# Kernel tuning notes

Hardware: AMD Instinct MI355X
Metric: run time of the kernel (lower is better)

The kernel has to match this reference:

```python
import jax, jax.numpy as jnp
import numpy as np

N_NODES = 100000
N_EDGES = 1600000


def gcn_conv(x, src, dst, W, b, n_nodes):
    # PyG GCNConv: h = x @ W; symmetric normalization with self-loops; scatter-add; + bias
    deg = jax.ops.segment_sum(jnp.ones_like(src, dtype=x.dtype), dst, num_segments=n_nodes)
    dinv = jax.lax.rsqrt(jnp.where(deg > 0, deg, 1.0))
    norm = dinv[src] * dinv[dst]              # [E+N]
    h = x @ W                                  # [N, out]
    msg = h[src] * norm[:, None]               # gather + scale (irregular access)
    out = jax.ops.segment_sum(msg, dst, num_segments=n_nodes)  # scatter-add aggregate
    return out + b


def setup_inputs() -> dict:
    key = jax.random.key(0)
    k1, k2, k3, k4 = jax.random.split(key, 4)
    x = jax.random.normal(k1, (N_NODES, 128), dtype=jnp.float32)
    edge_index = jax.random.randint(k2, (2, N_EDGES), 0, N_NODES, dtype=jnp.int64)
    W1 = jax.random.normal(k3, (128, 48), dtype=jnp.float32) * (1.0 / np.sqrt(128))
    b1 = jnp.zeros((48,), dtype=jnp.float32)
    W2 = jax.random.normal(k4, (48, 16), dtype=jnp.float32) * (1.0 / np.sqrt(48))
    b2 = jnp.zeros((16,), dtype=jnp.float32)
    return {"x": x, "edge_index": edge_index, "W1": W1, "b1": b1, "W2": W2, "b2": b2}


def reference(x, edge_index, W1, b1, W2, b2):
    n = x.shape[0]
    loops = jnp.arange(n, dtype=edge_index.dtype)
    src = jnp.concatenate([edge_index[0], loops])  # add self-loops
    dst = jnp.concatenate([edge_index[1], loops])
    h = gcn_conv(x, src, dst, W1, b1, n)
    h = jax.nn.relu(h)
    h = gcn_conv(h, src, dst, W2, b2, n)
    h = jax.nn.relu(h)
    return jax.nn.softmax(h, axis=1)
```

## Files before the change

### kernel.cpp

```cpp
#include <hip/hip_runtime.h>
#include <hip/hip_bf16.h>
#include <hip/hip_fp16.h>


#define TILE 4096

typedef _Float16 half8 __attribute__((ext_vector_type(8)));
typedef float floatx4 __attribute__((ext_vector_type(4)));

__global__ __launch_bounds__(256) void k_bhist(const int* __restrict__ dst, int E,
                                               int* __restrict__ Hw, int nbuck) {
    __shared__ int h[512];
    int t = threadIdx.x;
    for (int i = t; i < nbuck; i += 256) h[i] = 0;
    __syncthreads();
    int base = blockIdx.x * TILE;
#pragma unroll
    for (int r = 0; r < TILE / 256; ++r) {
        int e = base + r * 256 + t;
        if (e < E) atomicAdd(&h[dst[e] >> 8], 1);
    }
    __syncthreads();
    for (int i = t; i < nbuck; i += 256) Hw[blockIdx.x * nbuck + i] = h[i];
}

__global__ __launch_bounds__(256) void k_bsum(const int* __restrict__ Hw, int nTiles,
                                              int nbuck, int* __restrict__ btot) {
    int wid = (blockIdx.x * 256 + threadIdx.x) >> 6;
    int lane = threadIdx.x & 63;
    if (wid >= nbuck) return;
    int sum = 0;
    for (int tt = lane; tt < nTiles; tt += 64) sum += Hw[tt * nbuck + wid];
#pragma unroll
    for (int off = 32; off; off >>= 1) sum += __shfl_down(sum, off);
    if (lane == 0) btot[wid] = sum;
}

__global__ __launch_bounds__(512) void k_bscan2(const int* __restrict__ btot, int nbuck,
                                                int* __restrict__ bstart) {
    __shared__ int s[512];
    int t = threadIdx.x;
    int v = (t < nbuck) ? btot[t] : 0;
    s[t] = v;
    __syncthreads();
    for (int off = 1; off < 512; off <<= 1) {
        int tmp = (t >= off) ? s[t - off] : 0;
        __syncthreads();
        s[t] += tmp;
        __syncthreads();
    }
    if (t < nbuck) bstart[t] = s[t] - v;
    if (t == nbuck - 1) bstart[nbuck] = s[t];
}

__global__ __launch_bounds__(256) void k_boff(int* __restrict__ Hw, int nTiles,
                                              int nbuck, const int* __restrict__ bstart) {
    int wid = (blockIdx.x * 256 + threadIdx.x) >> 6;
    int lane = threadIdx.x & 63;
    if (wid >= nbuck) return;
    int running = bstart[wid];
    for (int chunk = 0; chunk < nTiles; chunk += 64) {
        int tt = chunk + lane;
        int v = (tt < nTiles) ? Hw[tt * nbuck + wid] : 0;
        int incl = v;
#pragma unroll
        for (int off = 1; off < 64; off <<= 1) {
            int u = __shfl_up(incl, off);
            if (lane >= off) incl += u;
        }
        if (tt < nTiles) Hw[tt * nbuck + wid] = running + (incl - v);
        running += __shfl(incl, 63);
    }
}

__global__ __launch_bounds__(256) void k_bscatter(const int* __restrict__ ei, int E,
                                                  const int* __restrict__ Hw, int nbuck,
                                                  int* __restrict__ ebuf) {
    __shared__ int cur[512];
    int t = threadIdx.x;
    for (int i = t; i < nbuck; i += 256) cur[i] = Hw[blockIdx.x * nbuck + i];
    __syncthreads();
    int base = blockIdx.x * TILE;
#pragma unroll
    for (int r = 0; r < TILE / 256; ++r) {
        int e = base + r * 256 + t;
        if (e < E) {
            int s = ei[e];
            int d = ei[E + e];
            int pos = atomicAdd(&cur[d >> 8], 1);
            ebuf[pos] = s | ((d & 255) << 17);
        }
    }
}

__global__ __launch_bounds__(256) void k_csrfill(const int* __restrict__ ebuf,
                                                 const int* __restrict__ bstart,
                                                 int* __restrict__ csr,
                                                 int* __restrict__ rowstart,
                                                 float* __restrict__ dinv, int N) {
    __shared__ int lcnt[256];
    __shared__ int lscan[256];
    __shared__ int lcur[256];
    int t = threadIdx.x;
    int nodebase = blockIdx.x << 8;
    int segs = bstart[blockIdx.x];
    int sege = bstart[blockIdx.x + 1];
    lcnt[t] = 0;
    __syncthreads();
    for (int i = segs + t; i < sege; i += 256)
        atomicAdd(&lcnt[((unsigned)ebuf[i]) >> 17], 1);
    __syncthreads();
    int v = lcnt[t];
    lscan[t] = v;
    __syncthreads();
    for (int off = 1; off < 256; off <<= 1) {
        int tmp = (t >= off) ? lscan[t - off] : 0;
        __syncthreads();
        lscan[t] += tmp;
        __syncthreads();
    }
    int excl = lscan[t] - v;
    int node = nodebase + t;
    int rs = segs + excl;
    if (node < N) {
        rowstart[node] = rs;
        dinv[node] = rsqrtf((float)(v + 1));
        if (node == N - 1) rowstart[N] = rs + v;
    }
    lcur[t] = rs;
    __syncthreads();
    for (int i = segs + t; i < sege; i += 256) {
        int pk = ebuf[i];
        int pos = atomicAdd(&lcur[((unsigned)pk) >> 17], 1);
        csr[pos] = pk & 0x1FFFF;
    }
}

__global__ __launch_bounds__(256) void k_gemm1(const float* __restrict__ x,
                                               const float* __restrict__ W1,
                                               const float* __restrict__ dinv,
                                               __half* __restrict__ h1p, int N) {
    __shared__ _Float16 wt[48 * 136];
    int t = threadIdx.x;
    for (int i = t; i < 128 * 48; i += 256) {
        int k = i / 48, c = i % 48;
        wt[c * 136 + k] = (_Float16)W1[i];
    }
    __syncthreads();

    int wave = t >> 6, lane = t & 63;
    int g = lane >> 4;
    int rtile = blockIdx.x * 64 + wave * 16;
    int rowA = rtile + (lane & 15);
    const float* xrow = x + (size_t)(rowA < N ? rowA : N - 1) * 128;
    int c0 = lane & 15;

    floatx4 acc[3];
#pragma unroll
    for (int nt = 0; nt < 3; ++nt)
#pragma unroll
        for (int q = 0; q < 4; ++q) acc[nt][q] = 0.f;

#pragma unroll
    for (int kc = 0; kc < 4; ++kc) {
        int k0 = kc * 32 + g * 8;
        float4 a0 = *(const float4*)(xrow + k0);
        float4 a1 = *(const float4*)(xrow + k0 + 4);
        half8 a;
        a[0] = (_Float16)a0.x; a[1] = (_Float16)a0.y;
        a[2] = (_Float16)a0.z; a[3] = (_Float16)a0.w;
        a[4] = (_Float16)a1.x; a[5] = (_Float16)a1.y;
        a[6] = (_Float16)a1.z; a[7] = (_Float16)a1.w;
#pragma unroll
        for (int nt = 0; nt < 3; ++nt) {
            half8 b = *(const half8*)(&wt[(nt * 16 + c0) * 136 + k0]);
            acc[nt] = __builtin_amdgcn_mfma_f32_16x16x32_f16(a, b, acc[nt], 0, 0, 0);
        }
    }

    int rbase = rtile + g * 4;
#pragma unroll
    for (int j = 0; j < 4; ++j) {
        int r = rbase + j;
        if (r < N) {
            float dr = dinv[r];
#pragma unroll
            for (int nt = 0; nt < 3; ++nt)
                h1p[(size_t)r * 48 + nt * 16 + c0] = __float2half(acc[nt][j] * dr);
        }
    }
}

__global__ __launch_bounds__(256) void k_agg1(const __half* __restrict__ h1p,
                                              const int* __restrict__ csr,
                                              const int* __restrict__ rowstart,
                                              const float* __restrict__ dinv,
                                              const float* __restrict__ b1,
                                              __half* __restrict__ r1h, int N) {
    int wave = threadIdx.x >> 6;
    int lane = threadIdx.x & 63;
    int v = blockIdx.x * 4 + wave;
    if (v >= N) return;
    int grp = lane >> 3;
    int sub = lane & 7;

    int start = rowstart[v];
    int d = rowstart[v + 1] - start;
    float dv = dinv[v];
    const int* cs = csr + start;
    const char* h1b = (const char*)h1p;

    float acc[8] = {0.f, 0.f, 0.f, 0.f, 0.f, 0.f, 0.f, 0.f};

    for (int base = 0; base < d; base += 64) {
        int sreg = (base + lane < d) ? cs[base + lane] : 0;
        int nb = min(64, d - base);
        for (int j = 0; j < 8 && j * 8 < nb; ++j) {
            int s = __shfl(sreg, j * 8 + grp);
            if (j * 8 + grp < nb && sub < 6) {
                float4 rv = *(const float4*)(h1b + (size_t)s * 96 + sub * 16);
                const __half2* hp = (const __half2*)&rv;
#pragma unroll
                for (int q = 0; q < 4; ++q) {
                    float2 f = __half22float2(hp[q]);
                    acc[q * 2] += f.x;
                    acc[q * 2 + 1] += f.y;
                }
            }
        }
    }
#pragma unroll
    for (int i = 0; i < 8; ++i) {
        acc[i] += __shfl_xor(acc[i], 8);
        acc[i] += __shfl_xor(acc[i], 16);
        acc[i] += __shfl_xor(acc[i], 32);
    }
    if (grp == 0 && sub < 6) {
        float4 sv = *(const float4*)(h1b + (size_t)v * 96 + sub * 16);
        const __half2* hp = (const __half2*)&sv;
        __half2 ob[4];
#pragma unroll
        for (int q = 0; q < 4; ++q) {
            float2 sf = __half22float2(hp[q]);
            int fi = sub * 8 + q * 2;
            float o0 = fmaxf(dv * (acc[q * 2] + sf.x) + b1[fi], 0.f);
            float o1 = fmaxf(dv * (acc[q * 2 + 1] + sf.y) + b1[fi + 1], 0.f);
            ob[q] = __floats2half2_rn(o0, o1);
        }
        *(float4*)((char*)r1h + (size_t)v * 96 + sub * 16) = *(const float4*)ob;
    }
}

__global__ __launch_bounds__(256) void k_gemm2(const __half* __restrict__ r1h,
                                               const float* __restrict__ W2,
                                               const float* __restrict__ dinv,
                                               __half* __restrict__ h2p, int N) {
    __shared__ float w2s[48 * 16];
    int t = threadIdx.x;
    for (int i = t; i < 768; i += 256) w2s[i] = W2[i];
    __syncthreads();
    int flat = blockIdx.x * 256 + t;
    int row = flat >> 2;
    int cg = (flat & 3) * 4;
    if (row >= N) return;
    float4 acc = make_float4(0.f, 0.f, 0.f, 0.f);
    const __half2* xr = (const __half2*)((const char*)r1h + (size_t)row * 96);
#pragma unroll 4
    for (int kk = 0; kk < 24; ++kk) {
        float2 a = __half22float2(xr[kk]);
        float4 b0 = *(const float4*)(w2s + (2 * kk) * 16 + cg);
        float4 b1v = *(const float4*)(w2s + (2 * kk + 1) * 16 + cg);
        acc.x += a.x * b0.x + a.y * b1v.x;
        acc.y += a.x * b0.y + a.y * b1v.y;
        acc.z += a.x * b0.z + a.y * b1v.z;
        acc.w += a.x * b0.w + a.y * b1v.w;
    }
    float dr = dinv[row];
    __half2 h01 = __floats2half2_rn(acc.x * dr, acc.y * dr);
    __half2 h23 = __floats2half2_rn(acc.z * dr, acc.w * dr);
    __half* dst = h2p + (size_t)row * 16 + cg;
    *(__half2*)(dst) = h01;
    *(__half2*)(dst + 2) = h23;
}

__global__ __launch_bounds__(256) void k_agg2(const __half* __restrict__ h2p,
                                              const int* __restrict__ csr,
                                              const int* __restrict__ rowstart,
                                              const float* __restrict__ dinv,
                                              const float* __restrict__ b2,
                                              float* __restrict__ out, int N) {
    int tid = threadIdx.x;
    int lane = tid & 63;
    int hf = lane >> 5;
    int l32 = lane & 31;
    int grp = l32 >> 1;
    int sub = lane & 1;
    int v = (blockIdx.x * 4 + (tid >> 6)) * 2 + hf;
    if (v >= N) return;

    int start = rowstart[v];
    int d = rowstart[v + 1] - start;
    float dv = dinv[v];
    const int* cs = csr + start;
    const char* h2b = (const char*)h2p;

    float acc[8] = {0.f, 0.f, 0.f, 0.f, 0.f, 0.f, 0.f, 0.f};

    for (int base = 0; base < d; base += 32) {
        int sreg = (base + l32 < d) ? cs[base + l32] : 0;
        int nb = min(32, d - base);
#pragma unroll
        for (int j = 0; j < 2; ++j) {
            int e = j * 16 + grp;
            int s = __shfl(sreg, (hf << 5) + e);
            if (e < nb) {
                float4 rv = *(const float4*)(h2b + (size_t)s * 32 + sub * 16);
                const __half2* hp = (const __half2*)&rv;
#pragma unroll
                for (int q = 0; q < 4; ++q) {
                    float2 f = __half22float2(hp[q]);
                    acc[q * 2] += f.x;
                    acc[q * 2 + 1] += f.y;
                }
            }
        }
    }
#pragma unroll
    for (int i = 0; i < 8; ++i) {
        acc[i] += __shfl_xor(acc[i], 2);
        acc[i] += __shfl_xor(acc[i], 4);
        acc[i] += __shfl_xor(acc[i], 8);
        acc[i] += __shfl_xor(acc[i], 16);
    }
    if (grp == 0) {
        float4 sv = *(const float4*)(h2b + (size_t)v * 32 + sub * 16);
        const __half2* hp = (const __half2*)&sv;
        float z[8];
#pragma unroll
        for (int q = 0; q < 4; ++q) {
            float2 f = __half22float2(hp[q]);
            z[q * 2]     = fmaxf(dv * (acc[q * 2] + f.x) + b2[sub * 8 + q * 2], 0.f);
            z[q * 2 + 1] = fmaxf(dv * (acc[q * 2 + 1] + f.y) + b2[sub * 8 + q * 2 + 1], 0.f);
        }
        float m8 = z[0];
#pragma unroll
        for (int i = 1; i < 8; ++i) m8 = fmaxf(m8, z[i]);
        float m = fmaxf(m8, __shfl_xor(m8, 1));
        float p[8];
        float s8 = 0.f;
#pragma unroll
        for (int i = 0; i < 8; ++i) { p[i] = __expf(z[i] - m); s8 += p[i]; }
        float inv = 1.f / (s8 + __shfl_xor(s8, 1));
        float4* dst = (float4*)(out + (size_t)v * 16 + sub * 8);
        dst[0] = make_float4(p[0] * inv, p[1] * inv, p[2] * inv, p[3] * inv);
        dst[1] = make_float4(p[4] * inv, p[5] * inv, p[6] * inv, p[7] * inv);
    }
}

extern "C" void kernel_launch(void* const* d_in, const int* in_sizes, int n_in,
                              void* d_out, int out_size, void* d_ws, size_t ws_size,
                              hipStream_t stream) {
    const float* x  = (const float*)d_in[0];
    const int*   ei = (const int*)d_in[1];
    const float* W1 = (const float*)d_in[2];
    const float* b1 = (const float*)d_in[3];
    const float* W2 = (const float*)d_in[4];
    const float* b2 = (const float*)d_in[5];
    float* out = (float*)d_out;

    int N = in_sizes[0] / 128;
    int E = in_sizes[1] / 2;
    int NBK = (N + 255) >> 8;
    int nTiles = (E + TILE - 1) / TILE;

    char* p = (char*)d_ws;
    auto alloc = [&](size_t bytes) -> char* {
        char* q = p;
        p += (bytes + 255) & ~(size_t)255;
        return q;
    };
    int*    rowstart = (int*)alloc((size_t)(N + 1) * 4);
    float*  dinv     = (float*)alloc((size_t)N * 4);
    int*    btot     = (int*)alloc((size_t)NBK * 4);
    int*    bstart   = (int*)alloc((size_t)(NBK + 1) * 4);
    int*    Hw       = (int*)alloc((size_t)nTiles * NBK * 4);
    int*    csr      = (int*)alloc((size_t)E * 4);
    size_t  ovl_sz   = (size_t)N * 48 * 2 > (size_t)E * 4 ? (size_t)N * 48 * 2
                                                          : (size_t)E * 4;
    char*   ovl      = alloc(ovl_sz);
    int*    ebuf     = (int*)ovl;
    __half* h1p      = (__half*)ovl;
    __half* r1h      = (__half*)alloc((size_t)N * 48 * 2);
    __half* h2p      = h1p;

    int wgBuck = (NBK + 3) / 4;

    hipLaunchKernelGGL(k_bhist, dim3(nTiles), dim3(256), 0, stream, ei + E, E, Hw, NBK);
    hipLaunchKernelGGL(k_bsum, dim3(wgBuck), dim3(256), 0, stream, Hw, nTiles, NBK, btot);
    hipLaunchKernelGGL(k_bscan2, dim3(1), dim3(512), 0, stream, btot, NBK, bstart);
    hipLaunchKernelGGL(k_boff, dim3(wgBuck), dim3(256), 0, stream, Hw, nTiles, NBK, bstart);
    hipLaunchKernelGGL(k_bscatter, dim3(nTiles), dim3(256), 0, stream, ei, E, Hw, NBK, ebuf);
    hipLaunchKernelGGL(k_csrfill, dim3(NBK), dim3(256), 0, stream,
                       ebuf, bstart, csr, rowstart, dinv, N);
    hipLaunchKernelGGL(k_gemm1, dim3((N + 63) / 64), dim3(256), 0, stream,
                       x, W1, dinv, h1p, N);
    hipLaunchKernelGGL(k_agg1, dim3((N + 3) / 4), dim3(256), 0, stream,
                       h1p, csr, rowstart, dinv, b1, r1h, N);
    hipLaunchKernelGGL(k_gemm2, dim3((N * 4 + 255) / 256), dim3(256), 0, stream,
                       r1h, W2, dinv, h2p, N);
    hipLaunchKernelGGL(k_agg2, dim3((N + 7) / 8), dim3(256), 0, stream,
                       h2p, csr, rowstart, dinv, b2, out, N);
}
```

Measured before the change: 143.7 us.

## Fuse layer-1 aggregation with layer-2 GEMM and fold bucket scan into offsets

Merges k_agg1 and k_gemm2 into one kernel. Each wave aggregates a node's 48-wide row, stages the ReLU output in shared memory and multiplies it by W2 straight away, so the r1h intermediate never goes to global memory and one launch disappears. h1p rows are padded from 48 to 64 halves (128 bytes) so all eight lanes of a gather group load aligned 16-byte chunks without the sub<6 mask. The padding raises gather traffic per neighbor by a third. The single-block k_bscan2 is removed: each k_boff wave now computes its own bucket prefix by summing btot, which adds redundant reads in exchange for one fewer launch.

```diff
diff --git a/kernel.cpp b/kernel.cpp
--- a/kernel.cpp
+++ b/kernel.cpp
@@ -36,29 +36,22 @@
     if (lane == 0) btot[wid] = sum;
 }
 
-__global__ __launch_bounds__(512) void k_bscan2(const int* __restrict__ btot, int nbuck,
-                                                int* __restrict__ bstart) {
-    __shared__ int s[512];
-    int t = threadIdx.x;
-    int v = (t < nbuck) ? btot[t] : 0;
-    s[t] = v;
-    __syncthreads();
-    for (int off = 1; off < 512; off <<= 1) {
-        int tmp = (t >= off) ? s[t - off] : 0;
-        __syncthreads();
-        s[t] += tmp;
-        __syncthreads();
-    }
-    if (t < nbuck) bstart[t] = s[t] - v;
-    if (t == nbuck - 1) bstart[nbuck] = s[t];
-}
-
 __global__ __launch_bounds__(256) void k_boff(int* __restrict__ Hw, int nTiles,
-                                              int nbuck, const int* __restrict__ bstart) {
+                                              int nbuck, const int* __restrict__ btot,
+                                              int* __restrict__ bstart) {
     int wid = (blockIdx.x * 256 + threadIdx.x) >> 6;
     int lane = threadIdx.x & 63;
     if (wid >= nbuck) return;
-    int running = bstart[wid];
+    int ps = 0;
+    for (int j = lane; j < wid; j += 64) ps += btot[j];
+#pragma unroll
+    for (int off = 32; off; off >>= 1) ps += __shfl_down(ps, off);
+    int prefix = __shfl(ps, 0);
+    if (lane == 0) {
+        bstart[wid] = prefix;
+        if (wid == nbuck - 1) bstart[nbuck] = prefix + btot[wid];
+    }
+    int running = prefix;
     for (int chunk = 0; chunk < nTiles; chunk += 64) {
         int tt = chunk + lane;
         int v = (tt < nTiles) ? Hw[tt * nbuck + wid] : 0;
@@ -186,101 +179,88 @@
             float dr = dinv[r];
 #pragma unroll
             for (int nt = 0; nt < 3; ++nt)
-                h1p[(size_t)r * 48 + nt * 16 + c0] = __float2half(acc[nt][j] * dr);
-        }
-    }
-}
-
-__global__ __launch_bounds__(256) void k_agg1(const __half* __restrict__ h1p,
-                                              const int* __restrict__ csr,
-                                              const int* __restrict__ rowstart,
-                                              const float* __restrict__ dinv,
-                                              const float* __restrict__ b1,
-                                              __half* __restrict__ r1h, int N) {
-    int wave = threadIdx.x >> 6;
-    int lane = threadIdx.x & 63;
+                h1p[(size_t)r * 64 + nt * 16 + c0] = __float2half(acc[nt][j] * dr);
+            h1p[(size_t)r * 64 + 48 + c0] = __float2half(0.f);
+        }
+    }
+}
+
+__global__ __launch_bounds__(256) void k_agg1f(const __half* __restrict__ h1p,
+                                               const int* __restrict__ csr,
+                                               const int* __restrict__ rowstart,
+                                               const float* __restrict__ dinv,
+                                               const float* __restrict__ b1,
+                                               const float* __restrict__ W2,
+                                               __half* __restrict__ h2p, int N) {
+    __shared__ float w2s[48 * 16];
+    __shared__ float r1s[4][48];
+    int t = threadIdx.x;
+    for (int i = t; i < 768; i += 256) w2s[i] = W2[i];
+
+    int wave = t >> 6;
+    int lane = t & 63;
     int v = blockIdx.x * 4 + wave;
-    if (v >= N) return;
+    bool active = v < N;
     int grp = lane >> 3;
     int sub = lane & 7;
 
-    int start = rowstart[v];
-    int d = rowstart[v + 1] - start;
-    float dv = dinv[v];
+    int start = 0, d = 0;
+    float dv = 0.f;
+    if (active) {
+        start = rowstart[v];
+        d = rowstart[v + 1] - start;
+        dv = dinv[v];
+    }
     const int* cs = csr + start;
     const char* h1b = (const char*)h1p;
 
     float acc[8] = {0.f, 0.f, 0.f, 0.f, 0.f, 0.f, 0.f, 0.f};
 
-    for (int base = 0; base < d; base += 64) {
-        int sreg = (base + lane < d) ? cs[base + lane] : 0;
-        int nb = min(64, d - base);
-        for (int j = 0; j < 8 && j * 8 < nb; ++j) {
-            int s = __shfl(sreg, j * 8 + grp);
-            if (j * 8 + grp < nb && sub < 6) {
-                float4 rv = *(const float4*)(h1b + (size_t)s * 96 + sub * 16);
-                const __half2* hp = (const __half2*)&rv;
-#pragma unroll
-                for (int q = 0; q < 4; ++q) {
-                    float2 f = __half22float2(hp[q]);
-                    acc[q * 2] += f.x;
-                    acc[q * 2 + 1] += f.y;
+    if (active) {
+        for (int base = 0; base < d; base += 64) {
+            int sreg = (base + lane < d) ? cs[base + lane] : 0;
+            int nb = min(64, d - base);
+#pragma unroll
+            for (int j = 0; j < 8; ++j) {
+                int e = j * 8 + grp;
+                int s = __shfl(sreg, e);
+                if (e < nb) {
+                    float4 rv = *(const float4*)(h1b + (size_t)s * 128 + sub * 16);
+                    const __half2* hp = (const __half2*)&rv;
+#pragma unroll
+                    for (int q = 0; q < 4; ++q) {
+                        float2 f = __half22float2(hp[q]);
+                        acc[q * 2] += f.x;
+                        acc[q * 2 + 1] += f.y;
+                    }
                 }
             }
         }
-    }
-#pragma unroll
-    for (int i = 0; i < 8; ++i) {
-        acc[i] += __shfl_xor(acc[i], 8);
-        acc[i] += __shfl_xor(acc[i], 16);
-        acc[i] += __shfl_xor(acc[i], 32);
-    }
-    if (grp == 0 && sub < 6) {
-        float4 sv = *(const float4*)(h1b + (size_t)v * 96 + sub * 16);
-        const __half2* hp = (const __half2*)&sv;
-        __half2 ob[4];
-#pragma unroll
-        for (int q = 0; q < 4; ++q) {
-            float2 sf = __half22float2(hp[q]);
-            int fi = sub * 8 + q * 2;
-            float o0 = fmaxf(dv * (acc[q * 2] + sf.x) + b1[fi], 0.f);
-            float o1 = fmaxf(dv * (acc[q * 2 + 1] + sf.y) + b1[fi + 1], 0.f);
-            ob[q] = __floats2half2_rn(o0, o1);
-        }
-        *(float4*)((char*)r1h + (size_t)v * 96 + sub * 16) = *(const float4*)ob;
-    }
-}
-
-__global__ __launch_bounds__(256) void k_gemm2(const __half* __restrict__ r1h,
-                                               const float* __restrict__ W2,
-                                               const float* __restrict__ dinv,
-                                               __half* __restrict__ h2p, int N) {
-    __shared__ float w2s[48 * 16];
-    int t = threadIdx.x;
-    for (int i = t; i < 768; i += 256) w2s[i] = W2[i];
-    __syncthreads();
-    int flat = blockIdx.x * 256 + t;
-    int row = flat >> 2;
-    int cg = (flat & 3) * 4;
-    if (row >= N) return;
-    float4 acc = make_float4(0.f, 0.f, 0.f, 0.f);
-    const __half2* xr = (const __half2*)((const char*)r1h + (size_t)row * 96);
-#pragma unroll 4
-    for (int kk = 0; kk < 24; ++kk) {
-        float2 a = __half22float2(xr[kk]);
-        float4 b0 = *(const float4*)(w2s + (2 * kk) * 16 + cg);
-        float4 b1v = *(const float4*)(w2s + (2 * kk + 1) * 16 + cg);
-        acc.x += a.x * b0.x + a.y * b1v.x;
-        acc.y += a.x * b0.y + a.y * b1v.y;
-        acc.z += a.x * b0.z + a.y * b1v.z;
-        acc.w += a.x * b0.w + a.y * b1v.w;
-    }
-    float dr = dinv[row];
-    __half2 h01 = __floats2half2_rn(acc.x * dr, acc.y * dr);
-    __half2 h23 = __floats2half2_rn(acc.z * dr, acc.w * dr);
-    __half* dst = h2p + (size_t)row * 16 + cg;
-    *(__half2*)(dst) = h01;
-    *(__half2*)(dst + 2) = h23;
+#pragma unroll
+        for (int i = 0; i < 8; ++i) {
+            acc[i] += __shfl_xor(acc[i], 8);
+            acc[i] += __shfl_xor(acc[i], 16);
+            acc[i] += __shfl_xor(acc[i], 32);
+        }
+        if (grp == 0 && sub < 6) {
+            float4 sv = *(const float4*)(h1b + (size_t)v * 128 + sub * 16);
+            const __half2* hp = (const __half2*)&sv;
+#pragma unroll
+            for (int q = 0; q < 4; ++q) {
+                float2 sf = __half22float2(hp[q]);
+                int fi = sub * 8 + q * 2;
+                r1s[wave][fi]     = fmaxf(dv * (acc[q * 2] + sf.x) + b1[fi], 0.f);
+                r1s[wave][fi + 1] = fmaxf(dv * (acc[q * 2 + 1] + sf.y) + b1[fi + 1], 0.f);
+            }
+        }
+    }
+    __syncthreads();
+    if (active && lane < 16) {
+        float s = 0.f;
+#pragma unroll 8
+        for (int k = 0; k < 48; ++k) s += r1s[wave][k] * w2s[k * 16 + lane];
+        h2p[(size_t)v * 16 + lane] = __float2half(s * dv);
+    }
 }
 
 __global__ __launch_bounds__(256) void k_agg2(const __half* __restrict__ h2p,
@@ -385,29 +365,26 @@
     int*    bstart   = (int*)alloc((size_t)(NBK + 1) * 4);
     int*    Hw       = (int*)alloc((size_t)nTiles * NBK * 4);
     int*    csr      = (int*)alloc((size_t)E * 4);
-    size_t  ovl_sz   = (size_t)N * 48 * 2 > (size_t)E * 4 ? (size_t)N * 48 * 2
-                                                          : (size_t)E * 4;
+    size_t  ovl_sz   = (size_t)N * 128 > (size_t)E * 4 ? (size_t)N * 128
+                                                       : (size_t)E * 4;
     char*   ovl      = alloc(ovl_sz);
     int*    ebuf     = (int*)ovl;
     __half* h1p      = (__half*)ovl;
-    __half* r1h      = (__half*)alloc((size_t)N * 48 * 2);
-    __half* h2p      = h1p;
+    __half* h2p      = (__half*)alloc((size_t)N * 16 * 2);
 
     int wgBuck = (NBK + 3) / 4;
 
     hipLaunchKernelGGL(k_bhist, dim3(nTiles), dim3(256), 0, stream, ei + E, E, Hw, NBK);
     hipLaunchKernelGGL(k_bsum, dim3(wgBuck), dim3(256), 0, stream, Hw, nTiles, NBK, btot);
-    hipLaunchKernelGGL(k_bscan2, dim3(1), dim3(512), 0, stream, btot, NBK, bstart);
-    hipLaunchKernelGGL(k_boff, dim3(wgBuck), dim3(256), 0, stream, Hw, nTiles, NBK, bstart);
+    hipLaunchKernelGGL(k_boff, dim3(wgBuck), dim3(256), 0, stream, Hw, nTiles, NBK,
+                       btot, bstart);
     hipLaunchKernelGGL(k_bscatter, dim3(nTiles), dim3(256), 0, stream, ei, E, Hw, NBK, ebuf);
     hipLaunchKernelGGL(k_csrfill, dim3(NBK), dim3(256), 0, stream,
                        ebuf, bstart, csr, rowstart, dinv, N);
     hipLaunchKernelGGL(k_gemm1, dim3((N + 63) / 64), dim3(256), 0, stream,
                        x, W1, dinv, h1p, N);
-    hipLaunchKernelGGL(k_agg1, dim3((N + 3) / 4), dim3(256), 0, stream,
-                       h1p, csr, rowstart, dinv, b1, r1h, N);
-    hipLaunchKernelGGL(k_gemm2, dim3((N * 4 + 255) / 256), dim3(256), 0, stream,
-                       r1h, W2, dinv, h2p, N);
+    hipLaunchKernelGGL(k_agg1f, dim3((N + 3) / 4), dim3(256), 0, stream,
+                       h1p, csr, rowstart, dinv, b1, W2, h2p, N);
     hipLaunchKernelGGL(k_agg2, dim3((N + 7) / 8), dim3(256), 0, stream,
                        h2p, csr, rowstart, dinv, b2, out, N);
 }
```

Result: slower. 160.8 us (+11.9%).
